# Performance work log

Measured on AMD Instinct MI355X. Metric: run time of the kernel, lower is better.

Reference implementation:

```python
import jax, jax.numpy as jnp
import numpy as np

D = 256
H1, H2 = 256, 128

def setup_inputs() -> dict:
    key0 = jax.random.key(0)
    ks = jax.random.split(key0, 10)
    B, Lq, Lk = 2, 512, 512
    query = jax.random.normal(ks[0], (B, Lq, D), dtype=jnp.float32)
    key_t = jax.random.normal(ks[1], (B, Lk, D), dtype=jnp.float32)
    value = jax.random.normal(ks[2], (B, Lk, D), dtype=jnp.float32)
    mask = jnp.ones((B, Lq, Lk), dtype=jnp.int32)
    s1 = 1.0 / np.sqrt(2 * D)
    W1 = jax.random.uniform(ks[3], (2 * D, H1), jnp.float32, -s1, s1)  # torch Linear(2D,H1), [in,out]
    b1 = jax.random.uniform(ks[4], (H1,), jnp.float32, -s1, s1)
    s2 = 1.0 / np.sqrt(H1)
    W2 = jax.random.uniform(ks[5], (H1, H2), jnp.float32, -s2, s2)
    b2 = jax.random.uniform(ks[6], (H2,), jnp.float32, -s2, s2)
    s3 = 1.0 / np.sqrt(H2)
    W3 = jax.random.uniform(ks[7], (H2, 1), jnp.float32, -s3, s3)
    b3 = jax.random.uniform(ks[8], (1,), jnp.float32, -s3, s3)
    return {"query": query, "key": key_t, "value": value, "mask": mask,
            "W1": W1, "b1": b1, "W2": W2, "b2": b2, "W3": W3, "b3": b3}

def reference(query, key, value, mask, W1, b1, W2, b2, W3, b3):
    # Original: cat([q_i, k_j]) @ W1 == q_i @ W1[:D] + k_j @ W1[D:]  (algebraic split,
    # identical math, avoids materializing the [B,Lq,Lk,2D] concat tensor).
    W1q, W1k = W1[:D], W1[D:]
    qp = jnp.einsum('bqd,dh->bqh', query, W1q)           # [B,Lq,H1]
    kp = jnp.einsum('bkd,dh->bkh', key, W1k)             # [B,Lk,H1]
    h1 = jax.nn.relu(qp[:, :, None, :] + kp[:, None, :, :] + b1)   # [B,Lq,Lk,H1]
    h2 = jax.nn.relu(jnp.einsum('bqkh,hj->bqkj', h1, W2) + b2)      # [B,Lq,Lk,H2]
    scores = (jnp.einsum('bqkj,jo->bqko', h2, W3) + b3)[..., 0]     # [B,Lq,Lk]
    scores = jnp.where(mask == 0, jnp.float32(-1e9), scores)
    attn = jax.nn.softmax(scores, axis=-1)               # dropout is identity in eval mode
    out = jnp.einsum('bqk,bkd->bqd', attn, value)
    return out, attn
```

## Files before the change

### kernel.cpp

```cpp
#include <hip/hip_runtime.h>

#define D_  256
#define H1_ 256
#define H2_ 128
#define B_  2
#define LQ_ 512
#define LK_ 512
#define BK  64

typedef float  f32x4  __attribute__((ext_vector_type(4)));
typedef __bf16 bf16x8 __attribute__((ext_vector_type(8)));
typedef __bf16 bf16x4 __attribute__((ext_vector_type(4)));

__global__ __launch_bounds__(512) void prep_kernel(
    const float* __restrict__ query, const float* __restrict__ key,
    const float* __restrict__ W1, const float* __restrict__ b1,
    const float* __restrict__ W2,
    float* __restrict__ qp, float* __restrict__ kp, __bf16* __restrict__ w2f) {
  const int blk = blockIdx.x;
  const int tid = threadIdx.x;
  if (blk >= 512) {
    const int id   = (blk - 512) * 512 + tid;
    const int j    = id & 7;
    const int lane = (id >> 3) & 63;
    const int frag = id >> 9;
    const int nt = frag & 3;
    const int wn = (frag >> 2) & 1;
    const int ks = (frag >> 3) & 1;
    const int kc = frag >> 4;
    const int n = wn * 64 + nt * 16 + (lane & 15);
    const int k = kc * 64 + ks * 32 + ((lane >> 4) << 3) + j;
    w2f[id] = (__bf16)W2[k * H2_ + n];
    return;
  }
  __shared__ float in_lds[4][D_];
  __shared__ float part[4][H1_];
  const int row0 = blk * 4;
  const int sel  = row0 >> 10;
  const float* __restrict__ src = sel ? key : query;
  const int base = (row0 & 1023) * D_;
  for (int i = tid; i < 4 * D_; i += 512)
    in_lds[i >> 8][i & 255] = src[base + i];
  __syncthreads();
  const int h  = tid & 255;
  const int kh = tid >> 8;
  float acc[4] = {0.f, 0.f, 0.f, 0.f};
  const float* __restrict__ w = W1 + sel * D_ * H1_ + kh * 128 * H1_ + h;
#pragma unroll 4
  for (int dd = 0; dd < 128; ++dd) {
    const float wv = w[dd * H1_];
    const int d = kh * 128 + dd;
#pragma unroll
    for (int r = 0; r < 4; ++r) acc[r] += in_lds[r][d] * wv;
  }
  if (kh == 1) {
#pragma unroll
    for (int r = 0; r < 4; ++r) part[r][h] = acc[r];
  }
  __syncthreads();
  if (kh == 0) {
    const float bias = sel ? 0.0f : b1[h];
    float* __restrict__ dst = sel ? kp : qp;
#pragma unroll
    for (int r = 0; r < 4; ++r)
      dst[base + r * H1_ + h] = acc[r] + part[r][h] + bias;
  }
}

__global__ __launch_bounds__(256, 2) void score_kernel(
    const float* __restrict__ qp, const float* __restrict__ kp,
    const __bf16* __restrict__ w2f,
    const float* __restrict__ b2, const float* __restrict__ W3,
    const float* __restrict__ b3, float* __restrict__ scores) {
  __shared__ __align__(16) __bf16 A_lds[128 * BK];
  __shared__ float  spart[2][128];

  const int b  = blockIdx.z;
  const int q0 = blockIdx.y * 8;
  const int k0 = blockIdx.x * 16;
  const int tid  = threadIdx.x;
  const int wave = tid >> 6;
  const int lane = tid & 63;
  const int quad = lane >> 4;
  const int l16  = lane & 15;
  const int wm   = wave >> 1;
  const int wn   = wave & 1;
  const int h8   = l16 & 7;

  const int qi = tid >> 5;
  const int t5 = (tid >> 4) & 1;
  const int kg = tid & 15;

  const float* __restrict__ qpb = qp + (b * LQ_ + q0) * H1_;
  const float* __restrict__ kpb = kp + (b * LK_ + k0) * H1_;

  f32x4 acc[4][4];
#pragma unroll
  for (int mt = 0; mt < 4; ++mt)
#pragma unroll
    for (int nt = 0; nt < 4; ++nt)
      acc[mt][nt] = (f32x4){0.f, 0.f, 0.f, 0.f};

  for (int kc = 0; kc < H1_ / BK; ++kc) {
    bf16x8 bfr[2][4];
#pragma unroll
    for (int ks = 0; ks < 2; ++ks)
#pragma unroll
      for (int nt = 0; nt < 4; ++nt)
        bfr[ks][nt] = *(const bf16x8*)(
            w2f + ((((kc * 2 + ks) * 2 + wn) * 4 + nt) * 64 + lane) * 8);

    const float4 qv = *(const float4*)(qpb + qi * H1_ + kc * BK + kg * 4);
#pragma unroll
    for (int ii = 0; ii < 8; ++ii) {
      const int ki = t5 * 8 + ii;
      const int r  = qi * 16 + ki;
      const float4 kv = *(const float4*)(kpb + ki * H1_ + kc * BK + kg * 4);
      bf16x4 a;
      a[0] = (__bf16)fmaxf(qv.x + kv.x, 0.f);
      a[1] = (__bf16)fmaxf(qv.y + kv.y, 0.f);
      a[2] = (__bf16)fmaxf(qv.z + kv.z, 0.f);
      a[3] = (__bf16)fmaxf(qv.w + kv.w, 0.f);
      const int sw = (((kg >> 1) ^ (r & 7)) << 3) + ((kg & 1) << 2);
      *(bf16x4*)(&A_lds[r * BK + sw]) = a;
    }
    __syncthreads();
#pragma unroll
    for (int ks = 0; ks < 2; ++ks) {
      const int cbase = ks * 4 + quad;
      bf16x8 af[4];
#pragma unroll
      for (int mt = 0; mt < 4; ++mt) {
        const int ra = wm * 64 + mt * 16 + l16;
        af[mt] = *(const bf16x8*)(&A_lds[ra * BK + ((cbase ^ h8) << 3)]);
      }
#pragma unroll
      for (int mt = 0; mt < 4; ++mt)
#pragma unroll
        for (int nt = 0; nt < 4; ++nt)
          acc[mt][nt] = __builtin_amdgcn_mfma_f32_16x16x32_bf16(
              af[mt], bfr[ks][nt], acc[mt][nt], 0, 0, 0);
    }
    __syncthreads();
  }

  float part[4][4];
#pragma unroll
  for (int mt = 0; mt < 4; ++mt)
#pragma unroll
    for (int rg = 0; rg < 4; ++rg) part[mt][rg] = 0.f;
#pragma unroll
  for (int nt = 0; nt < 4; ++nt) {
    const int col = wn * 64 + nt * 16 + l16;
    const float b2v = b2[col];
    const float w3v = W3[col];
#pragma unroll
    for (int mt = 0; mt < 4; ++mt)
#pragma unroll
      for (int rg = 0; rg < 4; ++rg) {
        float h2 = acc[mt][nt][rg] + b2v;
        h2 = fmaxf(h2, 0.f);
        part[mt][rg] += h2 * w3v;
      }
  }
#pragma unroll
  for (int off = 1; off < 16; off <<= 1)
#pragma unroll
    for (int mt = 0; mt < 4; ++mt)
#pragma unroll
      for (int rg = 0; rg < 4; ++rg)
        part[mt][rg] += __shfl_xor(part[mt][rg], off, 64);
  if (l16 == 0) {
#pragma unroll
    for (int mt = 0; mt < 4; ++mt)
#pragma unroll
      for (int rg = 0; rg < 4; ++rg) {
        const int rl = wm * 64 + mt * 16 + quad * 4 + rg;
        spart[wn][rl] = part[mt][rg];
      }
  }
  __syncthreads();
  if (tid < 128) {
    const float s = spart[0][tid] + spart[1][tid] + b3[0];
    const int qi2 = tid >> 4, ki2 = tid & 15;
    scores[(b * LQ_ + q0 + qi2) * LK_ + k0 + ki2] = s;
  }
}

__global__ __launch_bounds__(512) void smout_kernel(
    const float* __restrict__ sc, float* __restrict__ attn,
    const int* __restrict__ mask, const float* __restrict__ value,
    float* __restrict__ out) {
  const int qg = blockIdx.x, b = blockIdx.y;
  const int tid = threadIdx.x;
  __shared__ __align__(16) float a_lds[LK_][4];
  __shared__ __align__(16) f32x4 p_lds[7][4][64];
  const int row0 = b * LQ_ + qg * 4;
  const int w = tid >> 6, lane = tid & 63;
  if (w < 4) {
    const float* __restrict__ srow = sc + (row0 + w) * LK_;
    const int*  __restrict__ mrow = mask + (row0 + w) * LK_;
    float v[8];
#pragma unroll
    for (int j = 0; j < 8; ++j) {
      float s = srow[lane + j * 64];
      if (mrow[lane + j * 64] == 0) s = -1e9f;
      v[j] = s;
    }
    float m = v[0];
#pragma unroll
    for (int j = 1; j < 8; ++j) m = fmaxf(m, v[j]);
#pragma unroll
    for (int off = 32; off; off >>= 1) m = fmaxf(m, __shfl_xor(m, off, 64));
    float sum = 0.f;
#pragma unroll
    for (int j = 0; j < 8; ++j) { v[j] = __expf(v[j] - m); sum += v[j]; }
#pragma unroll
    for (int off = 32; off; off >>= 1) sum += __shfl_xor(sum, off, 64);
    const float inv = 1.f / sum;
    float* __restrict__ arow = attn + (row0 + w) * LK_;
#pragma unroll
    for (int j = 0; j < 8; ++j) {
      const float p = v[j] * inv;
      a_lds[lane + j * 64][w] = p;
      arow[lane + j * 64] = p;
    }
  }
  __syncthreads();
  const int kh2 = tid >> 6;
  const int dv  = tid & 63;
  f32x4 acc[4];
#pragma unroll
  for (int q = 0; q < 4; ++q) acc[q] = (f32x4){0.f, 0.f, 0.f, 0.f};
  const f32x4* __restrict__ vb4 = (const f32x4*)value + (b * LK_ + kh2 * 64) * 64 + dv;
#pragma unroll 4
  for (int k = 0; k < 64; ++k) {
    const f32x4 v4 = vb4[k * 64];
    const f32x4 p4 = *(const f32x4*)(&a_lds[kh2 * 64 + k][0]);
#pragma unroll
    for (int q = 0; q < 4; ++q) acc[q] += p4[q] * v4;
  }
  if (kh2 > 0) {
#pragma unroll
    for (int q = 0; q < 4; ++q) p_lds[kh2 - 1][q][dv] = acc[q];
  }
  __syncthreads();
  if (kh2 == 0) {
    f32x4* __restrict__ ob4 = (f32x4*)out + row0 * 64 + dv;
#pragma unroll
    for (int q = 0; q < 4; ++q) {
      f32x4 r = acc[q];
#pragma unroll
      for (int pp = 0; pp < 7; ++pp) r += p_lds[pp][q][dv];
      ob4[q * 64] = r;
    }
  }
}

extern "C" void kernel_launch(void* const* d_in, const int* in_sizes, int n_in,
                              void* d_out, int out_size, void* d_ws, size_t ws_size,
                              hipStream_t stream) {
  (void)in_sizes; (void)n_in; (void)out_size; (void)ws_size;
  const float* query = (const float*)d_in[0];
  const float* key   = (const float*)d_in[1];
  const float* value = (const float*)d_in[2];
  const int*   mask  = (const int*)d_in[3];
  const float* W1    = (const float*)d_in[4];
  const float* b1    = (const float*)d_in[5];
  const float* W2    = (const float*)d_in[6];
  const float* b2    = (const float*)d_in[7];
  const float* W3    = (const float*)d_in[8];
  const float* b3    = (const float*)d_in[9];

  float* out  = (float*)d_out;
  float* attn = out + B_ * LQ_ * D_;

  float*  qp  = (float*)d_ws;
  float*  kp  = qp + B_ * LQ_ * H1_;
  __bf16* w2f = (__bf16*)(kp + B_ * LK_ * H1_);
  float*  sc  = (float*)(w2f + H2_ * H1_);

  prep_kernel<<<576, 512, 0, stream>>>(query, key, W1, b1, W2, qp, kp, w2f);
  dim3 gscore(LK_ / 16, LQ_ / 8, B_);
  score_kernel<<<gscore, 256, 0, stream>>>(qp, kp, w2f, b2, W3, b3, sc);
  smout_kernel<<<dim3(128, B_), 512, 0, stream>>>(sc, attn, mask, value, out);
}
```

Before: 142.1 us.

## Build MFMA A-fragments in registers and stage full W2 in LDS for score kernel

The score kernel no longer writes the relu(qp+kp) tile to LDS through a swizzled layout with barriers per K-chunk. Each lane now forms its bf16 A fragment directly from qp/kp in registers. The whole bf16 W2 fragment array (64KB) is loaded into LDS once per block, and each wave owns 4 query rows across all 128 output columns, so the cross-wave score reduction goes away. Block size grows to 16x16 query-key pairs. The prep kernel is also retiled with float4 loads and 16 rows per block. In exchange, qp/kp are read from global or cache repeatedly, and the 64KB LDS use may limit occupancy.

```diff
diff --git a/kernel.cpp b/kernel.cpp
--- a/kernel.cpp
+++ b/kernel.cpp
@@ -6,21 +6,19 @@
 #define B_  2
 #define LQ_ 512
 #define LK_ 512
-#define BK  64
 
 typedef float  f32x4  __attribute__((ext_vector_type(4)));
 typedef __bf16 bf16x8 __attribute__((ext_vector_type(8)));
-typedef __bf16 bf16x4 __attribute__((ext_vector_type(4)));
-
-__global__ __launch_bounds__(512) void prep_kernel(
+
+__global__ __launch_bounds__(256) void prep_kernel(
     const float* __restrict__ query, const float* __restrict__ key,
     const float* __restrict__ W1, const float* __restrict__ b1,
     const float* __restrict__ W2,
     float* __restrict__ qp, float* __restrict__ kp, __bf16* __restrict__ w2f) {
   const int blk = blockIdx.x;
   const int tid = threadIdx.x;
-  if (blk >= 512) {
-    const int id   = (blk - 512) * 512 + tid;
+  if (blk >= 128) {
+    const int id   = (blk - 128) * 256 + tid;
     const int j    = id & 7;
     const int lane = (id >> 3) & 63;
     const int frag = id >> 9;
@@ -33,37 +31,44 @@
     w2f[id] = (__bf16)W2[k * H2_ + n];
     return;
   }
-  __shared__ float in_lds[4][D_];
-  __shared__ float part[4][H1_];
-  const int row0 = blk * 4;
+  __shared__ __align__(16) float part[16][H1_];
+  const int row0 = blk * 16;
   const int sel  = row0 >> 10;
-  const float* __restrict__ src = sel ? key : query;
-  const int base = (row0 & 1023) * D_;
-  for (int i = tid; i < 4 * D_; i += 512)
-    in_lds[i >> 8][i & 255] = src[base + i];
-  __syncthreads();
-  const int h  = tid & 255;
-  const int kh = tid >> 8;
-  float acc[4] = {0.f, 0.f, 0.f, 0.f};
-  const float* __restrict__ w = W1 + sel * D_ * H1_ + kh * 128 * H1_ + h;
-#pragma unroll 4
-  for (int dd = 0; dd < 128; ++dd) {
-    const float wv = w[dd * H1_];
-    const int d = kh * 128 + dd;
-#pragma unroll
-    for (int r = 0; r < 4; ++r) acc[r] += in_lds[r][d] * wv;
+  const float* __restrict__ src = (sel ? key : query) + (row0 & 1023) * D_;
+  const int hg = tid & 63;
+  const int rg = (tid >> 6) & 1;
+  const int kh = tid >> 7;
+  const float* __restrict__ w = W1 + sel * D_ * H1_ + kh * 128 * H1_ + hg * 4;
+  const float* __restrict__ x = src + rg * 8 * D_ + kh * 128;
+  f32x4 acc[8];
+#pragma unroll
+  for (int r = 0; r < 8; ++r) acc[r] = (f32x4){0.f, 0.f, 0.f, 0.f};
+  for (int dd = 0; dd < 128; dd += 4) {
+    f32x4 wv[4];
+#pragma unroll
+    for (int i = 0; i < 4; ++i) wv[i] = *(const f32x4*)(w + (dd + i) * H1_);
+#pragma unroll
+    for (int r = 0; r < 8; ++r) {
+      const f32x4 xv = *(const f32x4*)(x + r * D_ + dd);
+#pragma unroll
+      for (int i = 0; i < 4; ++i) acc[r] += xv[i] * wv[i];
+    }
   }
   if (kh == 1) {
 #pragma unroll
-    for (int r = 0; r < 4; ++r) part[r][h] = acc[r];
+    for (int r = 0; r < 8; ++r)
+      *(f32x4*)(&part[rg * 8 + r][hg * 4]) = acc[r];
   }
   __syncthreads();
   if (kh == 0) {
-    const float bias = sel ? 0.0f : b1[h];
-    float* __restrict__ dst = sel ? kp : qp;
-#pragma unroll
-    for (int r = 0; r < 4; ++r)
-      dst[base + r * H1_ + h] = acc[r] + part[r][h] + bias;
+    float* __restrict__ dst = (sel ? kp : qp) + (row0 & 1023) * H1_;
+    f32x4 bv = (f32x4){0.f, 0.f, 0.f, 0.f};
+    if (!sel) bv = *(const f32x4*)(b1 + hg * 4);
+#pragma unroll
+    for (int r = 0; r < 8; ++r) {
+      const f32x4 res = acc[r] + *(const f32x4*)(&part[rg * 8 + r][hg * 4]) + bv;
+      *(f32x4*)(dst + (rg * 8 + r) * H1_ + hg * 4) = res;
+    }
   }
 }
 
@@ -72,76 +77,65 @@
     const __bf16* __restrict__ w2f,
     const float* __restrict__ b2, const float* __restrict__ W3,
     const float* __restrict__ b3, float* __restrict__ scores) {
-  __shared__ __align__(16) __bf16 A_lds[128 * BK];
-  __shared__ float  spart[2][128];
+  __shared__ __align__(16) __bf16 w2lds[H1_ * H2_];
 
   const int b  = blockIdx.z;
-  const int q0 = blockIdx.y * 8;
+  const int q0 = blockIdx.y * 16;
   const int k0 = blockIdx.x * 16;
   const int tid  = threadIdx.x;
-  const int wave = tid >> 6;
+  const int wv   = tid >> 6;
   const int lane = tid & 63;
   const int quad = lane >> 4;
   const int l16  = lane & 15;
-  const int wm   = wave >> 1;
-  const int wn   = wave & 1;
-  const int h8   = l16 & 7;
-
-  const int qi = tid >> 5;
-  const int t5 = (tid >> 4) & 1;
-  const int kg = tid & 15;
-
-  const float* __restrict__ qpb = qp + (b * LQ_ + q0) * H1_;
-  const float* __restrict__ kpb = kp + (b * LK_ + k0) * H1_;
-
-  f32x4 acc[4][4];
+
+  {
+    const f32x4* __restrict__ s4 = (const f32x4*)w2f;
+    f32x4* d4 = (f32x4*)w2lds;
+#pragma unroll
+    for (int i = 0; i < 16; ++i)
+      d4[i * 256 + tid] = s4[i * 256 + tid];
+  }
+
+  f32x4 acc[4][8];
 #pragma unroll
   for (int mt = 0; mt < 4; ++mt)
 #pragma unroll
-    for (int nt = 0; nt < 4; ++nt)
+    for (int nt = 0; nt < 8; ++nt)
       acc[mt][nt] = (f32x4){0.f, 0.f, 0.f, 0.f};
 
-  for (int kc = 0; kc < H1_ / BK; ++kc) {
-    bf16x8 bfr[2][4];
-#pragma unroll
-    for (int ks = 0; ks < 2; ++ks)
-#pragma unroll
-      for (int nt = 0; nt < 4; ++nt)
-        bfr[ks][nt] = *(const bf16x8*)(
-            w2f + ((((kc * 2 + ks) * 2 + wn) * 4 + nt) * 64 + lane) * 8);
-
-    const float4 qv = *(const float4*)(qpb + qi * H1_ + kc * BK + kg * 4);
-#pragma unroll
-    for (int ii = 0; ii < 8; ++ii) {
-      const int ki = t5 * 8 + ii;
-      const int r  = qi * 16 + ki;
-      const float4 kv = *(const float4*)(kpb + ki * H1_ + kc * BK + kg * 4);
-      bf16x4 a;
-      a[0] = (__bf16)fmaxf(qv.x + kv.x, 0.f);
-      a[1] = (__bf16)fmaxf(qv.y + kv.y, 0.f);
-      a[2] = (__bf16)fmaxf(qv.z + kv.z, 0.f);
-      a[3] = (__bf16)fmaxf(qv.w + kv.w, 0.f);
-      const int sw = (((kg >> 1) ^ (r & 7)) << 3) + ((kg & 1) << 2);
-      *(bf16x4*)(&A_lds[r * BK + sw]) = a;
-    }
-    __syncthreads();
+  const float* __restrict__ qpb = qp + (b * LQ_ + q0 + wv * 4) * H1_ + quad * 8;
+  const float* __restrict__ kpb = kp + (b * LK_ + k0 + l16) * H1_ + quad * 8;
+
+  __syncthreads();
+
+#pragma unroll
+  for (int kc = 0; kc < 4; ++kc) {
 #pragma unroll
     for (int ks = 0; ks < 2; ++ks) {
-      const int cbase = ks * 4 + quad;
-      bf16x8 af[4];
+      const int col = kc * 64 + ks * 32;
+      const f32x4 kv0 = *(const f32x4*)(kpb + col);
+      const f32x4 kv1 = *(const f32x4*)(kpb + col + 4);
+      bf16x8 bfr[8];
+      const __bf16* fb = w2lds + (kc * 2 + ks) * 8 * 512 + lane * 8;
+#pragma unroll
+      for (int nt = 0; nt < 8; ++nt)
+        bfr[nt] = *(const bf16x8*)(fb + nt * 512);
 #pragma unroll
       for (int mt = 0; mt < 4; ++mt) {
-        const int ra = wm * 64 + mt * 16 + l16;
-        af[mt] = *(const bf16x8*)(&A_lds[ra * BK + ((cbase ^ h8) << 3)]);
+        const f32x4 qv0 = *(const f32x4*)(qpb + mt * H1_ + col);
+        const f32x4 qv1 = *(const f32x4*)(qpb + mt * H1_ + col + 4);
+        bf16x8 a;
+#pragma unroll
+        for (int jj = 0; jj < 4; ++jj) {
+          a[jj]     = (__bf16)fmaxf(qv0[jj] + kv0[jj], 0.f);
+          a[jj + 4] = (__bf16)fmaxf(qv1[jj] + kv1[jj], 0.f);
+        }
+#pragma unroll
+        for (int nt = 0; nt < 8; ++nt)
+          acc[mt][nt] = __builtin_amdgcn_mfma_f32_16x16x32_bf16(
+              a, bfr[nt], acc[mt][nt], 0, 0, 0);
       }
-#pragma unroll
-      for (int mt = 0; mt < 4; ++mt)
-#pragma unroll
-        for (int nt = 0; nt < 4; ++nt)
-          acc[mt][nt] = __builtin_amdgcn_mfma_f32_16x16x32_bf16(
-              af[mt], bfr[ks][nt], acc[mt][nt], 0, 0, 0);
-    }
-    __syncthreads();
+    }
   }
 
   float part[4][4];
@@ -150,18 +144,15 @@
 #pragma unroll
     for (int rg = 0; rg < 4; ++rg) part[mt][rg] = 0.f;
 #pragma unroll
-  for (int nt = 0; nt < 4; ++nt) {
-    const int col = wn * 64 + nt * 16 + l16;
-    const float b2v = b2[col];
-    const float w3v = W3[col];
+  for (int nt = 0; nt < 8; ++nt) {
+    const int cn = (nt >> 2) * 64 + (nt & 3) * 16 + l16;
+    const float b2v = b2[cn];
+    const float w3v = W3[cn];
 #pragma unroll
     for (int mt = 0; mt < 4; ++mt)
 #pragma unroll
-      for (int rg = 0; rg < 4; ++rg) {
-        float h2 = acc[mt][nt][rg] + b2v;
-        h2 = fmaxf(h2, 0.f);
-        part[mt][rg] += h2 * w3v;
-      }
+      for (int rg = 0; rg < 4; ++rg)
+        part[mt][rg] += fmaxf(acc[mt][nt][rg] + b2v, 0.f) * w3v;
   }
 #pragma unroll
   for (int off = 1; off < 16; off <<= 1)
@@ -171,19 +162,13 @@
       for (int rg = 0; rg < 4; ++rg)
         part[mt][rg] += __shfl_xor(part[mt][rg], off, 64);
   if (l16 == 0) {
+    const float b3v = b3[0];
 #pragma unroll
     for (int mt = 0; mt < 4; ++mt)
 #pragma unroll
-      for (int rg = 0; rg < 4; ++rg) {
-        const int rl = wm * 64 + mt * 16 + quad * 4 + rg;
-        spart[wn][rl] = part[mt][rg];
-      }
-  }
-  __syncthreads();
-  if (tid < 128) {
-    const float s = spart[0][tid] + spart[1][tid] + b3[0];
-    const int qi2 = tid >> 4, ki2 = tid & 15;
-    scores[(b * LQ_ + q0 + qi2) * LK_ + k0 + ki2] = s;
+      for (int rg = 0; rg < 4; ++rg)
+        scores[(b * LQ_ + q0 + wv * 4 + mt) * LK_ + k0 + quad * 4 + rg] =
+            part[mt][rg] + b3v;
   }
 }
 
@@ -280,8 +265,8 @@
   __bf16* w2f = (__bf16*)(kp + B_ * LK_ * H1_);
   float*  sc  = (float*)(w2f + H2_ * H1_);
 
-  prep_kernel<<<576, 512, 0, stream>>>(query, key, W1, b1, W2, qp, kp, w2f);
-  dim3 gscore(LK_ / 16, LQ_ / 8, B_);
+  prep_kernel<<<256, 256, 0, stream>>>(query, key, W1, b1, W2, qp, kp, w2f);
+  dim3 gscore(LK_ / 16, LQ_ / 16, B_);
   score_kernel<<<gscore, 256, 0, stream>>>(qp, kp, w2f, b2, W3, b3, sc);
   smout_kernel<<<dim3(128, B_), 512, 0, stream>>>(sc, attn, mask, value, out);
 }
```

Measured after the change: 175.1 us. 23.2% more time.

## Double-buffer hidden-activation tile in score kernel and vectorize prep LDS reads

Applied to the files above, without the earlier changes.

The score kernel now keeps two LDS buffers for the relu(qp+kp) bf16 tile. It builds the next H1 chunk while running MFMAs on the current one, so global loads and conversion overlap with matrix math, and each iteration drops one barrier. The prep kernel reads four input values at once as a float4 from LDS and loads four W1 values per step. The cost is double the LDS footprint in the score kernel, which could reduce occupancy, plus extra register pressure.

```diff
diff --git a/kernel.cpp b/kernel.cpp
--- a/kernel.cpp
+++ b/kernel.cpp
@@ -33,7 +33,7 @@
     w2f[id] = (__bf16)W2[k * H2_ + n];
     return;
   }
-  __shared__ float in_lds[4][D_];
+  __shared__ __align__(16) float in_lds[4][D_];
   __shared__ float part[4][H1_];
   const int row0 = blk * 4;
   const int sel  = row0 >> 10;
@@ -47,11 +47,17 @@
   float acc[4] = {0.f, 0.f, 0.f, 0.f};
   const float* __restrict__ w = W1 + sel * D_ * H1_ + kh * 128 * H1_ + h;
 #pragma unroll 4
-  for (int dd = 0; dd < 128; ++dd) {
-    const float wv = w[dd * H1_];
+  for (int dd = 0; dd < 128; dd += 4) {
+    float wv[4];
+#pragma unroll
+    for (int i = 0; i < 4; ++i) wv[i] = w[(dd + i) * H1_];
     const int d = kh * 128 + dd;
 #pragma unroll
-    for (int r = 0; r < 4; ++r) acc[r] += in_lds[r][d] * wv;
+    for (int r = 0; r < 4; ++r) {
+      const f32x4 xv = *(const f32x4*)(&in_lds[r][d]);
+#pragma unroll
+      for (int i = 0; i < 4; ++i) acc[r] += xv[i] * wv[i];
+    }
   }
   if (kh == 1) {
 #pragma unroll
@@ -72,7 +78,7 @@
     const __bf16* __restrict__ w2f,
     const float* __restrict__ b2, const float* __restrict__ W3,
     const float* __restrict__ b3, float* __restrict__ scores) {
-  __shared__ __align__(16) __bf16 A_lds[128 * BK];
+  __shared__ __align__(16) __bf16 A_lds[2][128 * BK];
   __shared__ float  spart[2][128];
 
   const int b  = blockIdx.z;
@@ -101,30 +107,52 @@
     for (int nt = 0; nt < 4; ++nt)
       acc[mt][nt] = (f32x4){0.f, 0.f, 0.f, 0.f};
 
-  for (int kc = 0; kc < H1_ / BK; ++kc) {
-    bf16x8 bfr[2][4];
-#pragma unroll
-    for (int ks = 0; ks < 2; ++ks)
-#pragma unroll
-      for (int nt = 0; nt < 4; ++nt)
-        bfr[ks][nt] = *(const bf16x8*)(
-            w2f + ((((kc * 2 + ks) * 2 + wn) * 4 + nt) * 64 + lane) * 8);
-
-    const float4 qv = *(const float4*)(qpb + qi * H1_ + kc * BK + kg * 4);
+  {
+    const float4 qv = *(const float4*)(qpb + qi * H1_ + kg * 4);
 #pragma unroll
     for (int ii = 0; ii < 8; ++ii) {
       const int ki = t5 * 8 + ii;
       const int r  = qi * 16 + ki;
-      const float4 kv = *(const float4*)(kpb + ki * H1_ + kc * BK + kg * 4);
+      const float4 kv = *(const float4*)(kpb + ki * H1_ + kg * 4);
       bf16x4 a;
       a[0] = (__bf16)fmaxf(qv.x + kv.x, 0.f);
       a[1] = (__bf16)fmaxf(qv.y + kv.y, 0.f);
       a[2] = (__bf16)fmaxf(qv.z + kv.z, 0.f);
       a[3] = (__bf16)fmaxf(qv.w + kv.w, 0.f);
       const int sw = (((kg >> 1) ^ (r & 7)) << 3) + ((kg & 1) << 2);
-      *(bf16x4*)(&A_lds[r * BK + sw]) = a;
-    }
-    __syncthreads();
+      *(bf16x4*)(&A_lds[0][r * BK + sw]) = a;
+    }
+  }
+  __syncthreads();
+
+#pragma unroll 1
+  for (int kc = 0; kc < 4; ++kc) {
+    const int cur = kc & 1;
+    bf16x8 bfr[2][4];
+#pragma unroll
+    for (int ks = 0; ks < 2; ++ks)
+#pragma unroll
+      for (int nt = 0; nt < 4; ++nt)
+        bfr[ks][nt] = *(const bf16x8*)(
+            w2f + ((((kc * 2 + ks) * 2 + wn) * 4 + nt) * 64 + lane) * 8);
+
+    if (kc < 3) {
+      const float4 qv = *(const float4*)(qpb + qi * H1_ + (kc + 1) * BK + kg * 4);
+#pragma unroll
+      for (int ii = 0; ii < 8; ++ii) {
+        const int ki = t5 * 8 + ii;
+        const int r  = qi * 16 + ki;
+        const float4 kv = *(const float4*)(kpb + ki * H1_ + (kc + 1) * BK + kg * 4);
+        bf16x4 a;
+        a[0] = (__bf16)fmaxf(qv.x + kv.x, 0.f);
+        a[1] = (__bf16)fmaxf(qv.y + kv.y, 0.f);
+        a[2] = (__bf16)fmaxf(qv.z + kv.z, 0.f);
+        a[3] = (__bf16)fmaxf(qv.w + kv.w, 0.f);
+        const int sw = (((kg >> 1) ^ (r & 7)) << 3) + ((kg & 1) << 2);
+        *(bf16x4*)(&A_lds[cur ^ 1][r * BK + sw]) = a;
+      }
+    }
+
 #pragma unroll
     for (int ks = 0; ks < 2; ++ks) {
       const int cbase = ks * 4 + quad;
@@ -132,7 +160,7 @@
 #pragma unroll
       for (int mt = 0; mt < 4; ++mt) {
         const int ra = wm * 64 + mt * 16 + l16;
-        af[mt] = *(const bf16x8*)(&A_lds[ra * BK + ((cbase ^ h8) << 3)]);
+        af[mt] = *(const bf16x8*)(&A_lds[cur][ra * BK + ((cbase ^ h8) << 3)]);
       }
 #pragma unroll
       for (int mt = 0; mt < 4; ++mt)
```

New measurement: 158.6 us. +11.6%, slower.

## Prefetch next qp/kp chunk into registers during MFMA and vectorize prep LDS reads

Applied to the files above, without the earlier changes.

The score kernel now loads the next H1 chunk of qp and kp into registers right after the LDS barrier, so global-load latency overlaps the MFMA work of the current chunk. The kc loop is fully unrolled, and s_setprio raises wave priority around the MFMA block. Separately, the prep kernel reads four inputs at a time as a float4 from LDS and batches four W1 loads per step. This raises register pressure in a kernel launched with launch_bounds(256,2), which could cause spills or lower occupancy.

```diff
diff --git a/kernel.cpp b/kernel.cpp
--- a/kernel.cpp
+++ b/kernel.cpp
@@ -33,7 +33,7 @@
     w2f[id] = (__bf16)W2[k * H2_ + n];
     return;
   }
-  __shared__ float in_lds[4][D_];
+  __shared__ __align__(16) float in_lds[4][D_];
   __shared__ float part[4][H1_];
   const int row0 = blk * 4;
   const int sel  = row0 >> 10;
@@ -47,11 +47,17 @@
   float acc[4] = {0.f, 0.f, 0.f, 0.f};
   const float* __restrict__ w = W1 + sel * D_ * H1_ + kh * 128 * H1_ + h;
 #pragma unroll 4
-  for (int dd = 0; dd < 128; ++dd) {
-    const float wv = w[dd * H1_];
+  for (int dd = 0; dd < 128; dd += 4) {
+    float wv[4];
+#pragma unroll
+    for (int i = 0; i < 4; ++i) wv[i] = w[(dd + i) * H1_];
     const int d = kh * 128 + dd;
 #pragma unroll
-    for (int r = 0; r < 4; ++r) acc[r] += in_lds[r][d] * wv;
+    for (int r = 0; r < 4; ++r) {
+      const f32x4 xv = *(const f32x4*)(&in_lds[r][d]);
+#pragma unroll
+      for (int i = 0; i < 4; ++i) acc[r] += xv[i] * wv[i];
+    }
   }
   if (kh == 1) {
 #pragma unroll
@@ -101,7 +107,14 @@
     for (int nt = 0; nt < 4; ++nt)
       acc[mt][nt] = (f32x4){0.f, 0.f, 0.f, 0.f};
 
-  for (int kc = 0; kc < H1_ / BK; ++kc) {
+  float4 qv = *(const float4*)(qpb + qi * H1_ + kg * 4);
+  float4 kvr[8];
+#pragma unroll
+  for (int ii = 0; ii < 8; ++ii)
+    kvr[ii] = *(const float4*)(kpb + (t5 * 8 + ii) * H1_ + kg * 4);
+
+#pragma unroll
+  for (int kc = 0; kc < 4; ++kc) {
     bf16x8 bfr[2][4];
 #pragma unroll
     for (int ks = 0; ks < 2; ++ks)
@@ -110,21 +123,28 @@
         bfr[ks][nt] = *(const bf16x8*)(
             w2f + ((((kc * 2 + ks) * 2 + wn) * 4 + nt) * 64 + lane) * 8);
 
-    const float4 qv = *(const float4*)(qpb + qi * H1_ + kc * BK + kg * 4);
 #pragma unroll
     for (int ii = 0; ii < 8; ++ii) {
       const int ki = t5 * 8 + ii;
       const int r  = qi * 16 + ki;
-      const float4 kv = *(const float4*)(kpb + ki * H1_ + kc * BK + kg * 4);
       bf16x4 a;
-      a[0] = (__bf16)fmaxf(qv.x + kv.x, 0.f);
-      a[1] = (__bf16)fmaxf(qv.y + kv.y, 0.f);
-      a[2] = (__bf16)fmaxf(qv.z + kv.z, 0.f);
-      a[3] = (__bf16)fmaxf(qv.w + kv.w, 0.f);
+      a[0] = (__bf16)fmaxf(qv.x + kvr[ii].x, 0.f);
+      a[1] = (__bf16)fmaxf(qv.y + kvr[ii].y, 0.f);
+      a[2] = (__bf16)fmaxf(qv.z + kvr[ii].z, 0.f);
+      a[3] = (__bf16)fmaxf(qv.w + kvr[ii].w, 0.f);
       const int sw = (((kg >> 1) ^ (r & 7)) << 3) + ((kg & 1) << 2);
       *(bf16x4*)(&A_lds[r * BK + sw]) = a;
     }
     __syncthreads();
+
+    if (kc < 3) {
+      qv = *(const float4*)(qpb + qi * H1_ + (kc + 1) * BK + kg * 4);
+#pragma unroll
+      for (int ii = 0; ii < 8; ++ii)
+        kvr[ii] = *(const float4*)(
+            kpb + (t5 * 8 + ii) * H1_ + (kc + 1) * BK + kg * 4);
+    }
+
 #pragma unroll
     for (int ks = 0; ks < 2; ++ks) {
       const int cbase = ks * 4 + quad;
@@ -134,12 +154,14 @@
         const int ra = wm * 64 + mt * 16 + l16;
         af[mt] = *(const bf16x8*)(&A_lds[ra * BK + ((cbase ^ h8) << 3)]);
       }
+      __builtin_amdgcn_s_setprio(1);
 #pragma unroll
       for (int mt = 0; mt < 4; ++mt)
 #pragma unroll
         for (int nt = 0; nt < 4; ++nt)
           acc[mt][nt] = __builtin_amdgcn_mfma_f32_16x16x32_bf16(
               af[mt], bfr[ks][nt], acc[mt][nt], 0, 0, 0);
+      __builtin_amdgcn_s_setprio(0);
     }
     __syncthreads();
   }
```

New measurement: 147.8 us. +4.0%, slower.
